# Kernel optimization log

Measured on AMD Instinct MI355X. Metric: run time of the kernel, lower is better.

## Reference

```python
import jax, jax.numpy as jnp
import numpy as np

B, HW, DIM, HEADS, HEAD_DIM, MLP_DIM, WS = 64, 56, 384, 12, 32, 1536, 7
INNER = HEADS * HEAD_DIM
NEG = -1e9


def _masks():
    ws, d = WS, WS // 2
    ul = np.zeros((ws * ws, ws * ws), np.float32)
    ul[-d * ws:, :-d * ws] = NEG
    ul[:-d * ws, -d * ws:] = NEG
    lr = np.zeros((ws, ws, ws, ws), np.float32)
    lr[:, -d:, :, :-d] = NEG
    lr[:, :-d, :, -d:] = NEG
    return jnp.asarray(ul), jnp.asarray(lr.reshape(ws * ws, ws * ws))


def _rel_indices():
    # pairwise relative 2D offsets between the ws*ws positions in a window
    idx = np.stack(np.meshgrid(np.arange(WS), np.arange(WS), indexing='ij'), -1).reshape(-1, 2)
    rel = idx[None, :, :] - idx[:, None, :] + (WS - 1)  # values in [0, 2*WS-2]
    return jnp.asarray(rel)


def _ln(x, g, b):
    m = x.mean(-1, keepdims=True)
    v = x.var(-1, keepdims=True)
    return (x - m) * jax.lax.rsqrt(v + 1e-5) * g + b


def _window_attention(x, w_qkv, pos_emb, w_out, b_out):
    b = x.shape[0]
    disp = WS // 2
    nw = HW // WS  # windows per side
    x = jnp.roll(x, (-disp, -disp), axis=(1, 2))  # cyclic shift
    qkv = x @ w_qkv  # [b, H, W, 3*inner]
    q, k, v = jnp.split(qkv, 3, axis=-1)

    def part(t):  # b (nw w1) (nw w2) (h d) -> b h (nw*nw) (w1*w2) d
        t = t.reshape(b, nw, WS, nw, WS, HEADS, HEAD_DIM)
        return t.transpose(0, 5, 1, 3, 2, 4, 6).reshape(b, HEADS, nw * nw, WS * WS, HEAD_DIM)

    q, k, v = part(q), part(k), part(v)
    dots = jnp.einsum('bhwid,bhwjd->bhwij', q, k) * (HEAD_DIM ** -0.5)
    rel = _rel_indices()
    dots = dots + pos_emb[rel[..., 0], rel[..., 1]]  # relative position bias
    ul, lr = _masks()
    dots = dots.at[:, :, -nw:].add(ul)            # bottom row of windows
    dots = dots.at[:, :, nw - 1::nw].add(lr)      # rightmost column of windows
    attn = jax.nn.softmax(dots, axis=-1)
    out = jnp.einsum('bhwij,bhwjd->bhwid', attn, v)
    # b h (nw nw) (w1 w2) d -> b (nw w1) (nw w2) (h d)
    out = out.reshape(b, HEADS, nw, nw, WS, WS, HEAD_DIM)
    out = out.transpose(0, 2, 4, 3, 5, 1, 6).reshape(b, HW, HW, INNER)
    out = out @ w_out + b_out
    return jnp.roll(out, (disp, disp), axis=(1, 2))  # cyclic back-shift


def swin_block(x, w_qkv, pos_emb, w_out, b_out, ln1_g, ln1_b, ln2_g, ln2_b,
               w_mlp1, b_mlp1, w_mlp2, b_mlp2):
    x = x + _window_attention(_ln(x, ln1_g, ln1_b), w_qkv, pos_emb, w_out, b_out)
    h = _ln(x, ln2_g, ln2_b)
    h = jax.nn.gelu(h @ w_mlp1 + b_mlp1) @ w_mlp2 + b_mlp2
    return x + h


def setup_inputs() -> dict:
    key = jax.random.key(0)
    ks = jax.random.split(key, 8)
    s = lambda fan_in: fan_in ** -0.5
    return {
        'x': jax.random.normal(ks[0], (B, HW, HW, DIM), jnp.float32),
        'w_qkv': jax.random.normal(ks[1], (DIM, 3 * INNER), jnp.float32) * s(DIM),
        'pos_emb': jax.random.normal(ks[2], (2 * WS - 1, 2 * WS - 1), jnp.float32),
        'w_out': jax.random.normal(ks[3], (INNER, DIM), jnp.float32) * s(INNER),
        'b_out': jnp.zeros((DIM,), jnp.float32),
        'ln1_g': jnp.ones((DIM,), jnp.float32),
        'ln1_b': jnp.zeros((DIM,), jnp.float32),
        'ln2_g': jnp.ones((DIM,), jnp.float32),
        'ln2_b': jnp.zeros((DIM,), jnp.float32),
        'w_mlp1': jax.random.normal(ks[4], (DIM, MLP_DIM), jnp.float32) * s(DIM),
        'b_mlp1': jnp.zeros((MLP_DIM,), jnp.float32),
        'w_mlp2': jax.random.normal(ks[5], (MLP_DIM, DIM), jnp.float32) * s(MLP_DIM),
        'b_mlp2': jnp.zeros((DIM,), jnp.float32),
    }


def reference(x, w_qkv, pos_emb, w_out, b_out, ln1_g, ln1_b, ln2_g, ln2_b,
              w_mlp1, b_mlp1, w_mlp2, b_mlp2):
    return swin_block(x, w_qkv, pos_emb, w_out, b_out, ln1_g, ln1_b, ln2_g, ln2_b,
                      w_mlp1, b_mlp1, w_mlp2, b_mlp2)
```

## Files before the change

### kernel.cpp

```cpp
#include <hip/hip_runtime.h>
#include <stdint.h>
#include <stddef.h>


typedef unsigned short u16;
typedef __attribute__((ext_vector_type(8))) short bf16x8;
typedef __attribute__((ext_vector_type(8))) unsigned short u16x8;
typedef __attribute__((ext_vector_type(4))) float f32x4;
typedef __attribute__((ext_vector_type(2))) float f32x2;

#define HW2 3136

__device__ __forceinline__ u16 f2bf(float f) {
    unsigned u = __float_as_uint(f);
    return (u16)((u + 0x7FFFu + ((u >> 16) & 1u)) >> 16);
}

__device__ __forceinline__ float bf2f(u16 u) {
    return __uint_as_float((unsigned)u << 16);
}

__device__ __forceinline__ f32x4 mfma16(bf16x8 a, bf16x8 b, f32x4 c) {
    return __builtin_amdgcn_mfma_f32_16x16x32_bf16(a, b, c, 0, 0, 0);
}

__device__ __forceinline__ void a_copy16(const void* g, void* l) {
    __builtin_amdgcn_global_load_lds((const __attribute__((address_space(1))) void*)g,
                                     (__attribute__((address_space(3))) void*)l, 16, 0, 0);
}

__device__ __forceinline__ f32x2 ld2(const float* p) { return *(const f32x2*)p; }
__device__ __forceinline__ f32x2 ld2(const u16* p) {
    const unsigned u = *(const unsigned*)p;
    f32x2 r;
    r.x = __uint_as_float(u << 16);
    r.y = __uint_as_float(u & 0xffff0000u);
    return r;
}

__device__ __forceinline__ int xcd_swizzle(int bid, int nwg) {
    const int xcd = bid & 7;
    const int i = bid >> 3;
    const int q = nwg >> 3;
    const int r = nwg & 7;
    const int base = (xcd < r) ? xcd * (q + 1) : r * (q + 1) + (xcd - r) * q;
    return base + i;
}

__global__ __launch_bounds__(256) void wtrans(const float* __restrict__ w,
                                              u16* __restrict__ wt, int K, int N) {
    long tid = (long)blockIdx.x * 256 + threadIdx.x;
    if (tid >= (long)K * N) return;
    int n = (int)(tid / K), k = (int)(tid % K);
    wt[tid] = f2bf(w[(long)k * N + n]);
}

__global__ __launch_bounds__(256) void prep_tab(const float* __restrict__ pe,
                                                float* __restrict__ tab) {
    int tid = blockIdx.x * 256 + threadIdx.x;
    if (tid >= 4 * 2401) return;
    int cb = tid / 2401, rem = tid % 2401;
    int i = rem / 49, j = rem % 49;
    int ix = i % 7, jx = j % 7;
    int iy = i / 7, jy = j / 7;
    float v = pe[(jy - iy + 6) * 13 + (jx - ix + 6)];
    if ((cb & 1) && ((i >= 28) != (j >= 28))) v += -1e9f;
    if ((cb & 2) && ((ix >= 4) != (jx >= 4))) v += -1e9f;
    tab[tid] = v;
}

template <int SHIFT, typename TIN>
__global__ __launch_bounds__(256) void ln_kernel(const TIN* __restrict__ in,
                                                 u16* __restrict__ out,
                                                 const float* __restrict__ gw,
                                                 const float* __restrict__ bw) {
    const int lane = threadIdx.x & 63;
    const int wave = threadIdx.x >> 6;
    const long t = (long)blockIdx.x * 4 + wave;
    const TIN* row = in + t * 384;
    f32x2 v0 = ld2(row + lane * 2);
    f32x2 v1 = ld2(row + 128 + lane * 2);
    f32x2 v2 = ld2(row + 256 + lane * 2);
    float s = v0.x + v0.y + v1.x + v1.y + v2.x + v2.y;
    float q = v0.x * v0.x + v0.y * v0.y + v1.x * v1.x + v1.y * v1.y + v2.x * v2.x + v2.y * v2.y;
#pragma unroll
    for (int m = 1; m < 64; m <<= 1) {
        s += __shfl_xor(s, m);
        q += __shfl_xor(q, m);
    }
    const float mean = s * (1.f / 384.f);
    const float rstd = rsqrtf(q * (1.f / 384.f) - mean * mean + 1e-5f);
    long orow = t;
    if (SHIFT) {
        long b = t / HW2;
        int rem = (int)(t % HW2);
        int y = rem / 56 - 3; if (y < 0) y += 56;
        int x = rem % 56 - 3; if (x < 0) x += 56;
        orow = b * HW2 + y * 56 + x;
    }
    u16* po = out + orow * 384;
#pragma unroll
    for (int p = 0; p < 3; p++) {
        f32x2 vv = (p == 0) ? v0 : ((p == 1) ? v1 : v2);
        f32x2 gg = *(const f32x2*)(gw + p * 128 + lane * 2);
        f32x2 bb = *(const f32x2*)(bw + p * 128 + lane * 2);
        float a0 = (vv.x - mean) * rstd * gg.x + bb.x;
        float a1 = (vv.y - mean) * rstd * gg.y + bb.y;
        unsigned pk = (unsigned)f2bf(a0) | ((unsigned)f2bf(a1) << 16);
        *(unsigned*)(po + p * 128 + lane * 2) = pk;
    }
}

template <int EPI>
__global__ __launch_bounds__(256, 4) void gemm_bf16(const u16* __restrict__ A,
                                                    const u16* __restrict__ Bt,
                                                    int N, int K,
                                                    const float* __restrict__ bias,
                                                    const void* residv,
                                                    float* outf, u16* outb) {
    __shared__ u16 Abuf[8192];
    __shared__ u16 Bbuf[8192];
    const int bid = xcd_swizzle(blockIdx.x, gridDim.x);
    const int ntiles = N >> 7;
    const long m0 = (long)(bid / ntiles) << 7;
    const int n0 = (bid % ntiles) << 7;
    const int lane = threadIdx.x & 63;
    const int wave = threadIdx.x >> 6;
    const int wr = (wave >> 1) << 6;
    const int wc = (wave & 1) << 6;
    const int lr = lane & 15;
    const int g  = lane >> 4;

    const u16* aP0; const u16* aP1; const u16* aP2; const u16* aP3;
    const u16* bP0; const u16* bP1; const u16* bP2; const u16* bP3;
    int d0, d1, d2, d3;
    {
#define STAGE_INIT(j, aP, bP, dd)                                          \
        {                                                                  \
            const int o = (((j << 2) + wave) << 10) + lane * 16;           \
            const int row = o >> 7;                                        \
            const int slot = (o >> 4) & 7;                                 \
            const int ce = ((slot ^ (row & 7)) << 3);                      \
            aP = A + (size_t)(m0 + row) * K + ce;                          \
            bP = Bt + (size_t)(n0 + row) * K + ce;                         \
            dd = o >> 1;                                                   \
        }
        STAGE_INIT(0, aP0, bP0, d0)
        STAGE_INIT(1, aP1, bP1, d1)
        STAGE_INIT(2, aP2, bP2, d2)
        STAGE_INIT(3, aP3, bP3, d3)
#undef STAGE_INIT
    }

    f32x4 acc[4][4];
#pragma unroll
    for (int i = 0; i < 4; i++)
#pragma unroll
        for (int j = 0; j < 4; j++) acc[i][j] = (f32x4){0.f, 0.f, 0.f, 0.f};

    for (int k0 = 0; k0 < K; k0 += 64) {
        __syncthreads();
        a_copy16(aP0, Abuf + d0); a_copy16(bP0, Bbuf + d0); aP0 += 64; bP0 += 64;
        a_copy16(aP1, Abuf + d1); a_copy16(bP1, Bbuf + d1); aP1 += 64; bP1 += 64;
        a_copy16(aP2, Abuf + d2); a_copy16(bP2, Bbuf + d2); aP2 += 64; bP2 += 64;
        a_copy16(aP3, Abuf + d3); a_copy16(bP3, Bbuf + d3); aP3 += 64; bP3 += 64;
        __syncthreads();
#pragma unroll
        for (int t = 0; t < 2; t++) {
            bf16x8 bfr[4];
#pragma unroll
            for (int ni = 0; ni < 4; ni++) {
                const int row = wc + ni * 16 + lr;
                const int slot = ((t << 2) + g) ^ (row & 7);
                bfr[ni] = *(const bf16x8*)(Bbuf + row * 64 + slot * 8);
            }
#pragma unroll
            for (int mi = 0; mi < 4; mi++) {
                const int row = wr + mi * 16 + lr;
                const int slot = ((t << 2) + g) ^ (row & 7);
                const bf16x8 af = *(const bf16x8*)(Abuf + row * 64 + slot * 8);
#pragma unroll
                for (int ni = 0; ni < 4; ni++)
                    acc[mi][ni] = mfma16(af, bfr[ni], acc[mi][ni]);
            }
        }
    }

    const float* residf = (const float*)residv;
    const u16*  residb  = (const u16*)residv;
    const int g4 = g << 2;
    float bs[4];
    if (EPI != 0) {
#pragma unroll
        for (int ni = 0; ni < 4; ni++) bs[ni] = bias[n0 + wc + ni * 16 + lr];
    }
#pragma unroll
    for (int mi = 0; mi < 4; mi++) {
#pragma unroll
        for (int r = 0; r < 4; r++) {
            const long m = m0 + wr + mi * 16 + g4 + r;
            long mo = m;
            if (EPI == 1) {
                long b = m / HW2;
                int rem = (int)(m % HW2);
                int y = rem / 56 + 3; if (y >= 56) y -= 56;
                int x = rem % 56 + 3; if (x >= 56) x -= 56;
                mo = b * HW2 + y * 56 + x;
            }
#pragma unroll
            for (int ni = 0; ni < 4; ni++) {
                const float v = acc[mi][ni][r];
                const int n = n0 + wc + ni * 16 + lr;
                if (EPI == 0) {
                    outb[(size_t)m * N + n] = f2bf(v);
                } else if (EPI == 1) {
                    const size_t o = (size_t)mo * 384 + n;
                    outb[o] = f2bf(residf[o] + v + bs[ni]);
                } else if (EPI == 2) {
                    const float gx = v + bs[ni];
                    const float y = 0.7978845608028654f * gx * (1.f + 0.044715f * gx * gx);
                    const float e = __expf(-2.f * y);
                    outb[(size_t)m * N + n] = f2bf(gx * __builtin_amdgcn_rcpf(1.f + e));
                } else {
                    const size_t o = (size_t)m * 384 + n;
                    outf[o] = bf2f(residb[o]) + v + bs[ni];
                }
            }
        }
    }
}

__global__ __launch_bounds__(256) void attn_kernel(const u16* __restrict__ qkv,
                                                   const float* __restrict__ tab,
                                                   u16* __restrict__ outa) {
    __shared__ u16 sVt[4][2304];
    __shared__ u16 sP[4][4608];
    const int lane = threadIdx.x & 63;
    const int wave = threadIdx.x >> 6;
    const int bid = blockIdx.x;
    const int hg = bid % 3;
    const int win = (bid / 3) & 63;
    const int b = bid / 192;
    const int wy = win >> 3, wx = win & 7;
    const int head = hg * 4 + wave;
    const long wbase = (long)b * HW2 + (long)wy * 392 + wx * 7;
    const int c = lane & 15, g = lane >> 4;
    const int kk = g << 3;

    u16* vt = sVt[wave];
    for (int i = lane; i < 2304; i += 64) vt[i] = 0;
    if (lane < 49) {
        const long mr = wbase + (lane / 7) * 56 + (lane % 7);
        const u16* vr = qkv + mr * 1152 + 768 + head * 32;
#pragma unroll
        for (int u = 0; u < 4; u++) {
            u16x8 vv = *(const u16x8*)(vr + u * 8);
#pragma unroll
            for (int e = 0; e < 8; e++) vt[(u * 8 + e) * 72 + lane] = vv[e];
        }
    }

    bf16x8 aq[4], bk[4];
#pragma unroll
    for (int mi = 0; mi < 4; mi++) {
        int t = mi * 16 + c; t = t > 48 ? 48 : t;
        const long mr = wbase + (t / 7) * 56 + (t % 7);
        aq[mi] = *(const bf16x8*)(qkv + mr * 1152 + head * 32 + kk);
    }
#pragma unroll
    for (int ni = 0; ni < 4; ni++) {
        int t = ni * 16 + c; t = t > 48 ? 48 : t;
        const long mr = wbase + (t / 7) * 56 + (t % 7);
        bk[ni] = *(const bf16x8*)(qkv + mr * 1152 + 384 + head * 32 + kk);
    }

    f32x4 sc[4][4];
#pragma unroll
    for (int i = 0; i < 4; i++)
#pragma unroll
        for (int j = 0; j < 4; j++) sc[i][j] = (f32x4){0.f, 0.f, 0.f, 0.f};
#pragma unroll
    for (int mi = 0; mi < 4; mi++)
#pragma unroll
        for (int ni = 0; ni < 4; ni++) sc[mi][ni] = mfma16(aq[mi], bk[ni], sc[mi][ni]);

    const float* tb = tab + (((wy == 7) ? 1 : 0) | ((wx == 7) ? 2 : 0)) * 2401;
#pragma unroll
    for (int mi = 0; mi < 4; mi++) {
#pragma unroll
        for (int r = 0; r < 4; r++) {
            int i = mi * 16 + (g << 2) + r;
            int ic = i > 48 ? 48 : i;
#pragma unroll
            for (int ni = 0; ni < 4; ni++) {
                int j = ni * 16 + c;
                float sv;
                if (j < 49)
                    sv = sc[mi][ni][r] * 0.17677669529663689f + tb[ic * 49 + j];
                else
                    sv = -3.0e38f;
                sc[mi][ni][r] = sv;
            }
        }
    }

    u16* pp = sP[wave];
#pragma unroll
    for (int mi = 0; mi < 4; mi++) {
#pragma unroll
        for (int r = 0; r < 4; r++) {
            float sm = fmaxf(fmaxf(sc[mi][0][r], sc[mi][1][r]),
                             fmaxf(sc[mi][2][r], sc[mi][3][r]));
            sm = fmaxf(sm, __shfl_xor(sm, 1));
            sm = fmaxf(sm, __shfl_xor(sm, 2));
            sm = fmaxf(sm, __shfl_xor(sm, 4));
            sm = fmaxf(sm, __shfl_xor(sm, 8));
            float p0 = __expf(sc[mi][0][r] - sm);
            float p1 = __expf(sc[mi][1][r] - sm);
            float p2 = __expf(sc[mi][2][r] - sm);
            float p3 = __expf(sc[mi][3][r] - sm);
            float ss = p0 + p1 + p2 + p3;
            ss += __shfl_xor(ss, 1);
            ss += __shfl_xor(ss, 2);
            ss += __shfl_xor(ss, 4);
            ss += __shfl_xor(ss, 8);
            const float ri = 1.f / ss;
            const int i = mi * 16 + (g << 2) + r;
            pp[i * 72 + c] = f2bf(p0 * ri);
            pp[i * 72 + 16 + c] = f2bf(p1 * ri);
            pp[i * 72 + 32 + c] = f2bf(p2 * ri);
            pp[i * 72 + 48 + c] = f2bf(p3 * ri);
        }
    }
    __syncthreads();

    f32x4 oc[4][2];
#pragma unroll
    for (int i = 0; i < 4; i++) {
        oc[i][0] = (f32x4){0.f, 0.f, 0.f, 0.f};
        oc[i][1] = (f32x4){0.f, 0.f, 0.f, 0.f};
    }
#pragma unroll
    for (int ks = 0; ks < 2; ks++) {
        bf16x8 bv0 = *(const bf16x8*)(vt + c * 72 + kk + ks * 32);
        bf16x8 bv1 = *(const bf16x8*)(vt + (16 + c) * 72 + kk + ks * 32);
#pragma unroll
        for (int mi = 0; mi < 4; mi++) {
            bf16x8 ap = *(const bf16x8*)(pp + (mi * 16 + c) * 72 + kk + ks * 32);
            oc[mi][0] = mfma16(ap, bv0, oc[mi][0]);
            oc[mi][1] = mfma16(ap, bv1, oc[mi][1]);
        }
    }

#pragma unroll
    for (int mi = 0; mi < 4; mi++) {
#pragma unroll
        for (int r = 0; r < 4; r++) {
            const int i = mi * 16 + (g << 2) + r;
            if (i < 49) {
                const long mr = wbase + (i / 7) * 56 + (i % 7);
                u16* po = outa + mr * 384 + head * 32;
                po[c] = f2bf(oc[mi][0][r]);
                po[16 + c] = f2bf(oc[mi][1][r]);
            }
        }
    }
}

extern "C" void kernel_launch(void* const* d_in, const int* in_sizes, int n_in,
                              void* d_out, int out_size, void* d_ws, size_t ws_size,
                              hipStream_t stream) {
    (void)in_sizes; (void)n_in; (void)out_size;
    const float* x     = (const float*)d_in[0];
    const float* w_qkv = (const float*)d_in[1];
    const float* pos   = (const float*)d_in[2];
    const float* w_out = (const float*)d_in[3];
    const float* b_out = (const float*)d_in[4];
    const float* ln1g  = (const float*)d_in[5];
    const float* ln1b  = (const float*)d_in[6];
    const float* ln2g  = (const float*)d_in[7];
    const float* ln2b  = (const float*)d_in[8];
    const float* w1    = (const float*)d_in[9];
    const float* b1    = (const float*)d_in[10];
    const float* w2    = (const float*)d_in[11];
    const float* b2    = (const float*)d_in[12];
    float* out = (float*)d_out;
    char* ws = (char*)d_ws;

    u16* wqkvT  = (u16*)(ws + 0);
    u16* woutT  = (u16*)(ws + 884736);
    u16* wm1T   = (u16*)(ws + 1179648);
    u16* wm2T   = (u16*)(ws + 2359296);
    float* tab  = (float*)(ws + 3538944);
    const size_t pool0 = 3577856;
    const size_t avail = (ws_size > pool0) ? ws_size - pool0 : 0;

    int CH = 8;
    while (CH > 2 && (size_t)CH * 3136 * 4608ULL > avail) CH >>= 1;
    const int nchunks = 64 / CH;
    const int rows = CH * HW2;
    const int tiles = rows >> 7;
    u16* bufA = (u16*)(ws + pool0);
    u16* bufB = bufA + (size_t)rows * 384;
    u16* bufC = bufB + (size_t)rows * 1152;
    u16* bufD = bufC + (size_t)rows * 384;

    wtrans<<<1728, 256, 0, stream>>>(w_qkv, wqkvT, 384, 1152);
    wtrans<<<576, 256, 0, stream>>>(w_out, woutT, 384, 384);
    wtrans<<<2304, 256, 0, stream>>>(w1, wm1T, 384, 1536);
    wtrans<<<2304, 256, 0, stream>>>(w2, wm2T, 1536, 384);
    prep_tab<<<38, 256, 0, stream>>>(pos, tab);

    for (int c = 0; c < nchunks; ++c) {
        const float* xc = x + (size_t)c * rows * 384;
        float* oc = out + (size_t)c * rows * 384;
        ln_kernel<1, float><<<rows / 4, 256, 0, stream>>>(xc, bufA, ln1g, ln1b);
        gemm_bf16<0><<<tiles * 9, 256, 0, stream>>>(bufA, wqkvT, 1152, 384,
                                                    nullptr, nullptr, nullptr, bufB);
        attn_kernel<<<CH * 192, 256, 0, stream>>>(bufB, tab, bufC);
        gemm_bf16<1><<<tiles * 3, 256, 0, stream>>>(bufC, woutT, 384, 384,
                                                    b_out, xc, nullptr, bufD);
        ln_kernel<0, u16><<<rows / 4, 256, 0, stream>>>(bufD, bufA, ln2g, ln2b);
        gemm_bf16<2><<<tiles * 12, 256, 0, stream>>>(bufA, wm1T, 1536, 384,
                                                     b1, nullptr, nullptr, bufB);
        gemm_bf16<3><<<tiles * 3, 256, 0, stream>>>(bufB, wm2T, 384, 1536,
                                                    b2, bufD, oc, nullptr);
    }
}
```

Before: 1.570 ms.

## Double-buffer GEMM LDS tiles with BK=32 to overlap global loads with MFMA

Replaces the single-buffered 64-wide K tile with two 32-wide LDS buffers. The next tile is prefetched while the current one is consumed, using explicit vmcnt waits and raw barriers. The LDS swizzle is reworked for 32-element rows. The aim is to hide global-to-LDS latency behind MFMA work. The cost is twice as many loop iterations and barriers, and the hand-written waitcnt logic depends on how a_copy16 is implemented.

```diff
diff --git a/kernel.cpp b/kernel.cpp
--- a/kernel.cpp
+++ b/kernel.cpp
@@ -118,8 +118,8 @@
                                                     const float* __restrict__ bias,
                                                     const void* residv,
                                                     float* outf, u16* outb) {
-    __shared__ u16 Abuf[8192];
-    __shared__ u16 Bbuf[8192];
+    __shared__ u16 Abuf[2][4096];
+    __shared__ u16 Bbuf[2][4096];
     const int bid = xcd_swizzle(blockIdx.x, gridDim.x);
     const int ntiles = N >> 7;
     const long m0 = (long)(bid / ntiles) << 7;
@@ -131,25 +131,21 @@
     const int lr = lane & 15;
     const int g  = lane >> 4;
 
-    const u16* aP0; const u16* aP1; const u16* aP2; const u16* aP3;
-    const u16* bP0; const u16* bP1; const u16* bP2; const u16* bP3;
-    int d0, d1, d2, d3;
+    const u16 *aP0, *aP1, *bP0, *bP1;
+    int d0, d1;
     {
-#define STAGE_INIT(j, aP, bP, dd)                                          \
-        {                                                                  \
-            const int o = (((j << 2) + wave) << 10) + lane * 16;           \
-            const int row = o >> 7;                                        \
-            const int slot = (o >> 4) & 7;                                 \
-            const int ce = ((slot ^ (row & 7)) << 3);                      \
-            aP = A + (size_t)(m0 + row) * K + ce;                          \
-            bP = Bt + (size_t)(n0 + row) * K + ce;                         \
-            dd = o >> 1;                                                   \
-        }
-        STAGE_INIT(0, aP0, bP0, d0)
-        STAGE_INIT(1, aP1, bP1, d1)
-        STAGE_INIT(2, aP2, bP2, d2)
-        STAGE_INIT(3, aP3, bP3, d3)
-#undef STAGE_INIT
+        const int o0 = (wave << 10) + lane * 16;
+        const int r0 = o0 >> 6;
+        const int ce0 = (((o0 >> 4) & 3) ^ ((r0 >> 1) & 3)) << 3;
+        aP0 = A + (size_t)(m0 + r0) * K + ce0;
+        bP0 = Bt + (size_t)(n0 + r0) * K + ce0;
+        d0 = o0 >> 1;
+        const int o1 = ((4 + wave) << 10) + lane * 16;
+        const int r1 = o1 >> 6;
+        const int ce1 = (((o1 >> 4) & 3) ^ ((r1 >> 1) & 3)) << 3;
+        aP1 = A + (size_t)(m0 + r1) * K + ce1;
+        bP1 = Bt + (size_t)(n0 + r1) * K + ce1;
+        d1 = o1 >> 1;
     }
 
     f32x4 acc[4][4];
@@ -158,32 +154,44 @@
 #pragma unroll
         for (int j = 0; j < 4; j++) acc[i][j] = (f32x4){0.f, 0.f, 0.f, 0.f};
 
-    for (int k0 = 0; k0 < K; k0 += 64) {
-        __syncthreads();
-        a_copy16(aP0, Abuf + d0); a_copy16(bP0, Bbuf + d0); aP0 += 64; bP0 += 64;
-        a_copy16(aP1, Abuf + d1); a_copy16(bP1, Bbuf + d1); aP1 += 64; bP1 += 64;
-        a_copy16(aP2, Abuf + d2); a_copy16(bP2, Bbuf + d2); aP2 += 64; bP2 += 64;
-        a_copy16(aP3, Abuf + d3); a_copy16(bP3, Bbuf + d3); aP3 += 64; bP3 += 64;
-        __syncthreads();
-#pragma unroll
-        for (int t = 0; t < 2; t++) {
-            bf16x8 bfr[4];
-#pragma unroll
-            for (int ni = 0; ni < 4; ni++) {
-                const int row = wc + ni * 16 + lr;
-                const int slot = ((t << 2) + g) ^ (row & 7);
-                bfr[ni] = *(const bf16x8*)(Bbuf + row * 64 + slot * 8);
-            }
-#pragma unroll
-            for (int mi = 0; mi < 4; mi++) {
-                const int row = wr + mi * 16 + lr;
-                const int slot = ((t << 2) + g) ^ (row & 7);
-                const bf16x8 af = *(const bf16x8*)(Abuf + row * 64 + slot * 8);
-#pragma unroll
-                for (int ni = 0; ni < 4; ni++)
-                    acc[mi][ni] = mfma16(af, bfr[ni], acc[mi][ni]);
-            }
-        }
+    a_copy16(aP0, &Abuf[0][d0]); a_copy16(bP0, &Bbuf[0][d0]);
+    a_copy16(aP1, &Abuf[0][d1]); a_copy16(bP1, &Bbuf[0][d1]);
+    aP0 += 32; aP1 += 32; bP0 += 32; bP1 += 32;
+
+    const int nt = K >> 5;
+    int cur = 0;
+    for (int t = 0; t < nt; ++t) {
+        if (t + 1 < nt) {
+            a_copy16(aP0, &Abuf[cur ^ 1][d0]); a_copy16(bP0, &Bbuf[cur ^ 1][d0]);
+            a_copy16(aP1, &Abuf[cur ^ 1][d1]); a_copy16(bP1, &Bbuf[cur ^ 1][d1]);
+            aP0 += 32; aP1 += 32; bP0 += 32; bP1 += 32;
+            asm volatile("s_waitcnt vmcnt(4)" ::: "memory");
+        } else {
+            asm volatile("s_waitcnt vmcnt(0)" ::: "memory");
+        }
+        __builtin_amdgcn_s_barrier();
+        __builtin_amdgcn_sched_barrier(0);
+        bf16x8 af[4], bfr[4];
+#pragma unroll
+        for (int mi = 0; mi < 4; mi++) {
+            const int row = wr + mi * 16 + lr;
+            const int slot = g ^ ((row >> 1) & 3);
+            af[mi] = *(const bf16x8*)(&Abuf[cur][row * 32 + slot * 8]);
+        }
+#pragma unroll
+        for (int ni = 0; ni < 4; ni++) {
+            const int row = wc + ni * 16 + lr;
+            const int slot = g ^ ((row >> 1) & 3);
+            bfr[ni] = *(const bf16x8*)(&Bbuf[cur][row * 32 + slot * 8]);
+        }
+#pragma unroll
+        for (int mi = 0; mi < 4; mi++)
+#pragma unroll
+            for (int ni = 0; ni < 4; ni++)
+                acc[mi][ni] = mfma16(af[mi], bfr[ni], acc[mi][ni]);
+        __builtin_amdgcn_sched_barrier(0);
+        __builtin_amdgcn_s_barrier();
+        cur ^= 1;
     }
 
     const float* residf = (const float*)residv;
```

New measurement: 1.754 ms. +11.7%, slower.
